# Optimization experiments

Measured on AMD Instinct MI355X. Metric: run time of the kernel, lower is better.

Reference implementation:

```python
import jax, jax.numpy as jnp
import numpy as np
import math

B, T, D = 2, 1024, 4096
H, KVH = 32, 8
HD = D // H            # 128
GROUP = H // KVH       # 4
MAX_SEQ = 4096
ROPE_BASE = 10000.0


def rotate_every_two(x):
    # (x0,x1,x2,x3,...) -> (-x1,x0,-x3,x2,...)
    x1 = x[..., ::2]
    x2 = x[..., 1::2]
    return jnp.stack((-x2, x1), axis=-1).reshape(x.shape)


def build_rope_cache():
    inv_freq = 1.0 / (ROPE_BASE ** (jnp.arange(0, HD, 2, dtype=jnp.float32) / HD))
    t = jnp.arange(MAX_SEQ, dtype=jnp.float32)
    freqs = jnp.einsum('i,j->ij', t, inv_freq)        # (MAX_SEQ, HD/2)
    emb = jnp.concatenate([freqs, freqs], axis=-1)    # (MAX_SEQ, HD) -- matches torch cat([freqs,freqs])
    return jnp.cos(emb), jnp.sin(emb)


def setup_inputs() -> dict:
    key = jax.random.key(0)
    kx, kq, kk, kv, ko = jax.random.split(key, 5)
    x = jax.random.normal(kx, (B, T, D), dtype=jnp.float32)
    # weights stored (in_features, out_features)
    wq = jax.random.normal(kq, (D, H * HD), dtype=jnp.float32) * 0.02
    wk = jax.random.normal(kk, (D, KVH * HD), dtype=jnp.float32) * 0.02
    wv = jax.random.normal(kv, (D, KVH * HD), dtype=jnp.float32) * 0.02
    wo = jax.random.normal(ko, (H * HD, D), dtype=jnp.float32) * 0.02
    return {"x": x, "wq": wq, "wk": wk, "wv": wv, "wo": wo, "start_pos": 0}


def reference(x, wq, wk, wv, wo, start_pos):
    cos_cache, sin_cache = build_rope_cache()
    pos = start_pos + jnp.arange(T)
    cos_t = cos_cache[pos][None, None]   # (1,1,T,HD)
    sin_t = sin_cache[pos][None, None]

    q = (x @ wq).reshape(B, T, H, HD).transpose(0, 2, 1, 3)     # (B,H,T,HD)
    k = (x @ wk).reshape(B, T, KVH, HD).transpose(0, 2, 1, 3)   # (B,KVH,T,HD)
    v = (x @ wv).reshape(B, T, KVH, HD).transpose(0, 2, 1, 3)

    q = q * cos_t + rotate_every_two(q) * sin_t
    k = k * cos_t + rotate_every_two(k) * sin_t

    # GQA: repeat-interleave KV heads to match query heads
    k_exp = jnp.repeat(k, GROUP, axis=1)  # (B,H,T,HD)
    v_exp = jnp.repeat(v, GROUP, axis=1)

    scores = jnp.einsum('bhqd,bhkd->bhqk', q, k_exp) / math.sqrt(HD)
    # causal mask (T_q == T_k here): forbid k > q
    mask = jnp.arange(T)[None, :] > jnp.arange(T)[:, None]
    scores = jnp.where(mask[None, None], -jnp.inf, scores)
    attn = jax.nn.softmax(scores, axis=-1)

    out = jnp.einsum('bhqk,bhkd->bhqd', attn, v_exp)
    out = out.transpose(0, 2, 1, 3).reshape(B, T, H * HD)
    return out @ wo
```

## Files before the change

kernel.cpp:

```cpp
#include <hip/hip_runtime.h>
#include <hip/hip_bf16.h>
#include <math.h>

#define B_    2
#define T_    1024
#define D_    4096
#define H_    32
#define KVH_  8
#define HD_   128
#define GROUP_ 4

static constexpr float SCORE_SCALE = 0.08838834764831845f;

typedef __bf16 bf16x8 __attribute__((ext_vector_type(8)));
typedef float  f32x4  __attribute__((ext_vector_type(4)));
typedef unsigned short u16;

__device__ inline float toF(const __hip_bfloat16 v) { return __bfloat162float(v); }
__device__ inline float toF(const float v)          { return v; }

__device__ inline void storeC(float* p, float v)          { *p = v; }
__device__ inline void storeC(__hip_bfloat16* p, float v) { *p = __float2bfloat16(v); }

__device__ inline unsigned short f2bf(float f) {
    union { float f; unsigned u; } v; v.f = f;
    unsigned r = v.u + 0x7FFFu + ((v.u >> 16) & 1u);
    return (unsigned short)(r >> 16);
}

__device__ inline float bf2f(u16 u) {
    union { float f; unsigned u; } v; v.u = (unsigned)u << 16; return v.f;
}

__device__ inline void gload_lds16(const u16* g, u16* l) {
    __builtin_amdgcn_global_load_lds(
        (const __attribute__((address_space(1))) void*)g,
        (__attribute__((address_space(3))) void*)l, 16, 0, 0);
}


__global__ __launch_bounds__(256) void lconv(const float* __restrict__ S,
                                             u16* __restrict__ D, int n8) {
    int i = blockIdx.x * 256 + threadIdx.x;
    if (i >= n8) return;
    const float4 a = *(const float4*)(S + (size_t)i * 8);
    const float4 b = *(const float4*)(S + (size_t)i * 8 + 4);
    union { int4 v; u16 u[8]; } t;
    t.u[0] = f2bf(a.x); t.u[1] = f2bf(a.y); t.u[2] = f2bf(a.z); t.u[3] = f2bf(a.w);
    t.u[4] = f2bf(b.x); t.u[5] = f2bf(b.y); t.u[6] = f2bf(b.z); t.u[7] = f2bf(b.w);
    *(int4*)(D + (size_t)i * 8) = t.v;
}

template <bool DUAL>
__global__ __launch_bounds__(256) void tconv(const float* __restrict__ S0,
                                             u16* __restrict__ D0,
                                             const float* __restrict__ S1,
                                             u16* __restrict__ D1,
                                             int R, int Cc) {
    const float* __restrict__ S = (DUAL && blockIdx.z) ? S1 : S0;
    u16* __restrict__ D         = (DUAL && blockIdx.z) ? D1 : D0;
    __shared__ u16 Tt[64][72];
    const int tid = threadIdx.x;
    const int r0 = blockIdx.y * 64, c0 = blockIdx.x * 64;
    {
        const int rr = tid >> 4, cc4 = (tid & 15) * 4;
#pragma unroll
        for (int e = 0; e < 4; ++e) {
            const int row = rr + e * 16;
            float4 v = *(const float4*)(S + (size_t)(r0 + row) * Cc + c0 + cc4);
            union { int2 w; u16 u[4]; } t;
            t.u[0] = f2bf(v.x); t.u[1] = f2bf(v.y); t.u[2] = f2bf(v.z); t.u[3] = f2bf(v.w);
            *(int2*)&Tt[row][cc4] = t.w;
        }
    }
    __syncthreads();
    {
        const int cc = tid >> 2, r8 = (tid & 3) * 8;
#pragma unroll
        for (int e = 0; e < 2; ++e) {
            const int rb = r8 + e * 32;
            union { int4 v; u16 u[8]; } t;
#pragma unroll
            for (int j = 0; j < 8; ++j) t.u[j] = Tt[rb + j][cc];
            *(int4*)(D + (size_t)(c0 + cc) * R + r0 + rb) = t.v;
        }
    }
}

template <typename TC, bool DUAL, bool TRC1>
__global__ __launch_bounds__(256, 2) void gemm_bf16(const u16* __restrict__ A,
                                                    const u16* __restrict__ Bt0,
                                                    TC* __restrict__ C0,
                                                    const u16* __restrict__ Bt1,
                                                    TC* __restrict__ C1,
                                                    int M, int N, int K) {
    const u16* __restrict__ Bt = (DUAL && blockIdx.z) ? Bt1 : Bt0;
    TC* __restrict__ C         = (DUAL && blockIdx.z) ? C1 : C0;

    __shared__ u16 As[128 * 32];
    __shared__ u16 Bs[128 * 32];

    const int tid   = threadIdx.x;
    const int lane  = tid & 63;
    const int w     = tid >> 6;
    const int waveM = w >> 1;
    const int waveN = w & 1;
    const int lm    = lane & 15;
    const int quad  = lane >> 4;
    const int bm    = blockIdx.y * 128;
    const int bn    = blockIdx.x * 128;

    const int srow = w * 16 + (lane >> 2);
    const int scol = (lane & 3) * 8;

    const u16* agp0 = A  + (size_t)(bm + srow)      * K + scol;
    const u16* agp1 = A  + (size_t)(bm + srow + 64) * K + scol;
    const u16* bgp0 = Bt + (size_t)(bn + srow)      * K + scol;
    const u16* bgp1 = Bt + (size_t)(bn + srow + 64) * K + scol;

    u16* al0 = &As[(w * 16)      * 32];
    u16* al1 = &As[(w * 16 + 64) * 32];
    u16* bl0 = &Bs[(w * 16)      * 32];
    u16* bl1 = &Bs[(w * 16 + 64) * 32];

    f32x4 acc[4][4];
#pragma unroll
    for (int i = 0; i < 4; ++i)
#pragma unroll
        for (int j = 0; j < 4; ++j) acc[i][j] = (f32x4){0.f, 0.f, 0.f, 0.f};

    for (int k0 = 0; k0 < K; k0 += 32) {
        gload_lds16(agp0 + k0, al0);
        gload_lds16(agp1 + k0, al1);
        gload_lds16(bgp0 + k0, bl0);
        gload_lds16(bgp1 + k0, bl1);
        __syncthreads();

        bf16x8 af[4], bfv[4];
#pragma unroll
        for (int i = 0; i < 4; ++i)
            af[i] = *(const bf16x8*)&As[(waveM * 64 + i * 16 + lm) * 32 + quad * 8];
#pragma unroll
        for (int j = 0; j < 4; ++j)
            bfv[j] = *(const bf16x8*)&Bs[(waveN * 64 + j * 16 + lm) * 32 + quad * 8];
#pragma unroll
        for (int i = 0; i < 4; ++i)
#pragma unroll
            for (int j = 0; j < 4; ++j)
                acc[i][j] = __builtin_amdgcn_mfma_f32_16x16x32_bf16(af[i], bfv[j], acc[i][j], 0, 0, 0);
        __syncthreads();
    }

    if (TRC1 && DUAL && blockIdx.z) {
#pragma unroll
        for (int i = 0; i < 4; ++i) {
            int row0 = bm + waveM * 64 + i * 16 + quad * 4;
#pragma unroll
            for (int j = 0; j < 4; ++j) {
                int col = bn + waveN * 64 + j * 16 + lm;
#pragma unroll
                for (int rr = 0; rr < 4; ++rr)
                    storeC(&C[(size_t)col * M + row0 + rr], acc[i][j][rr]);
            }
        }
    } else {
#pragma unroll
        for (int i = 0; i < 4; ++i) {
            int row0 = bm + waveM * 64 + i * 16 + quad * 4;
#pragma unroll
            for (int j = 0; j < 4; ++j) {
                int col = bn + waveN * 64 + j * 16 + lm;
#pragma unroll
                for (int rr = 0; rr < 4; ++rr)
                    storeC(&C[(size_t)(row0 + rr) * N + col], acc[i][j][rr]);
            }
        }
    }
}

#define LSTR 40

template <typename TA, typename TB, typename TC, bool DUAL, bool TRC1>
__global__ __launch_bounds__(256) void gemm_mfma(const TA* __restrict__ A,
                                                 const TB* __restrict__ B0,
                                                 TC* __restrict__ C0,
                                                 const TB* __restrict__ B1,
                                                 TC* __restrict__ C1,
                                                 int M, int N, int K) {
    const TB* __restrict__ B = (DUAL && blockIdx.z) ? B1 : B0;
    TC* __restrict__ C       = (DUAL && blockIdx.z) ? C1 : C0;

    __shared__ unsigned short As[128 * LSTR];
    __shared__ unsigned short Bs[128 * LSTR];

    const int tid   = threadIdx.x;
    const int lane  = tid & 63;
    const int wv    = tid >> 6;
    const int waveM = wv >> 1;
    const int waveN = wv & 1;
    const int lm    = lane & 15;
    const int quad  = lane >> 4;
    const int bm    = blockIdx.y * 128;
    const int bn    = blockIdx.x * 128;

    f32x4 acc[4][4];
#pragma unroll
    for (int i = 0; i < 4; ++i)
#pragma unroll
        for (int j = 0; j < 4; ++j) acc[i][j] = (f32x4){0.f, 0.f, 0.f, 0.f};

    for (int k0 = 0; k0 < K; k0 += 32) {
#pragma unroll
        for (int e = 0; e < 8; ++e) {
            int p  = tid + e * 256;
            int r  = p >> 4, c2 = (p & 15) * 2;
            const TA* ap = A + (size_t)(bm + r) * K + k0 + c2;
            ushort2 t;
            t.x = f2bf(toF(ap[0]));
            t.y = f2bf(toF(ap[1]));
            *(ushort2*)&As[r * LSTR + c2] = t;
        }
#pragma unroll
        for (int e = 0; e < 8; ++e) {
            int p  = tid + e * 256;
            int n  = p & 127, k2 = (p >> 7) * 2;
            const TB* bp = B + (size_t)(k0 + k2) * N + bn + n;
            ushort2 t;
            t.x = f2bf(toF(bp[0]));
            t.y = f2bf(toF(bp[N]));
            *(ushort2*)&Bs[n * LSTR + k2] = t;
        }
        __syncthreads();

        bf16x8 af[4], bfr[4];
#pragma unroll
        for (int i = 0; i < 4; ++i)
            af[i] = *(const bf16x8*)&As[(waveM * 64 + i * 16 + lm) * LSTR + quad * 8];
#pragma unroll
        for (int j = 0; j < 4; ++j)
            bfr[j] = *(const bf16x8*)&Bs[(waveN * 64 + j * 16 + lm) * LSTR + quad * 8];
#pragma unroll
        for (int i = 0; i < 4; ++i)
#pragma unroll
            for (int j = 0; j < 4; ++j)
                acc[i][j] = __builtin_amdgcn_mfma_f32_16x16x32_bf16(af[i], bfr[j], acc[i][j], 0, 0, 0);
        __syncthreads();
    }

    if (TRC1 && DUAL && blockIdx.z) {
#pragma unroll
        for (int i = 0; i < 4; ++i) {
            int row0 = bm + waveM * 64 + i * 16 + quad * 4;
#pragma unroll
            for (int j = 0; j < 4; ++j) {
                int col = bn + waveN * 64 + j * 16 + lm;
#pragma unroll
                for (int rr = 0; rr < 4; ++rr)
                    storeC(&C[(size_t)col * M + row0 + rr], acc[i][j][rr]);
            }
        }
    } else {
#pragma unroll
        for (int i = 0; i < 4; ++i) {
            int row0 = bm + waveM * 64 + i * 16 + quad * 4;
#pragma unroll
            for (int j = 0; j < 4; ++j) {
                int col = bn + waveN * 64 + j * 16 + lm;
#pragma unroll
                for (int rr = 0; rr < 4; ++rr)
                    storeC(&C[(size_t)(row0 + rr) * N + col], acc[i][j][rr]);
            }
        }
    }
}

__device__ inline void rope_apply8(__hip_bfloat16* p, const float* cs,
                                   const float* sn, int t0) {
    union { int4 v; u16 u[8]; } in, outv;
    in.v = *(const int4*)p;
    float x[8];
#pragma unroll
    for (int i = 0; i < 8; ++i) x[i] = bf2f(in.u[i]);
#pragma unroll
    for (int pr = 0; pr < 4; ++pr) {
        float c0 = cs[t0 + 2 * pr],     s0 = sn[t0 + 2 * pr];
        float c1 = cs[t0 + 2 * pr + 1], s1 = sn[t0 + 2 * pr + 1];
        float e = x[2 * pr], o = x[2 * pr + 1];
        outv.u[2 * pr]     = f2bf(e * c0 - o * s0);
        outv.u[2 * pr + 1] = f2bf(o * c1 + e * s1);
    }
    *(int4*)p = outv.v;
}

__global__ __launch_bounds__(256) void rope_tok(__hip_bfloat16* __restrict__ Q,
                                                __hip_bfloat16* __restrict__ K,
                                                const int* __restrict__ start_pos) {
    __shared__ float cs[64], sn[64];
    const int n   = blockIdx.x;
    const int tid = threadIdx.x;
    const int pos = *start_pos + (n % T_);

    if (tid < 64) {
        float invf = exp2f(-(float)tid * 0.20762050593045232f);
        float ang  = (float)pos * invf;
        float s, c;
        __sincosf(ang, &s, &c);
        s = sinf(ang); c = cosf(ang);
        cs[tid] = c; sn[tid] = s;
    }
    __syncthreads();

    __hip_bfloat16* qrow = Q + (size_t)n * (H_ * HD_);
    __hip_bfloat16* krow = K + (size_t)n * (KVH_ * HD_);
#pragma unroll
    for (int e = 0; e < 2; ++e) {
        int g = tid + e * 256;
        rope_apply8(qrow + g * 8, cs, sn, (g * 8) & 63);
    }
    if (tid < 128)
        rope_apply8(krow + tid * 8, cs, sn, (tid * 8) & 63);
}

template <typename TQ, typename TK>
__global__ __launch_bounds__(256) void rope_kernel(TQ* __restrict__ Q,
                                                   TK* __restrict__ Kt,
                                                   const int* __restrict__ start_pos) {
    int w    = blockIdx.x * 4 + (threadIdx.x >> 6);
    int lane = threadIdx.x & 63;
    int hh = w % (H_ + KVH_);
    int n  = w / (H_ + KVH_);
    int t  = n % T_;
    int pos = *start_pos + t;

    int e0 = 2 * lane, e1 = 2 * lane + 1;
    int j0 = e0 & 63,  j1 = e1 & 63;
    const double LN_BASE = 9.210340371976184;
    double a0 = (double)pos * exp(-((double)(2 * j0) / 128.0) * LN_BASE);
    double a1 = (double)pos * exp(-((double)(2 * j1) / 128.0) * LN_BASE);
    float c0 = (float)cos(a0), s0 = (float)sin(a0);
    float c1 = (float)cos(a1), s1 = (float)sin(a1);

    if (hh < H_) {
        TQ* base = Q + (size_t)n * (H_ * HD_) + hh * HD_;
        float x0 = toF(base[e0]), x1 = toF(base[e1]);
        storeC(&base[e0], x0 * c0 - x1 * s0);
        storeC(&base[e1], x1 * c1 + x0 * s1);
    } else {
        TK* base = Kt + (size_t)n * (KVH_ * HD_) + (hh - H_) * HD_;
        float x0 = toF(base[e0]), x1 = toF(base[e1]);
        storeC(&base[e0], x0 * c0 - x1 * s0);
        storeC(&base[e1], x1 * c1 + x0 * s1);
    }
}

#define KSTR 136
#define VSTR 72
#define PSTR 72

template <typename TQ>
__global__ __launch_bounds__(256, 2) void flash_attn(
        const TQ* __restrict__ Q,
        const __hip_bfloat16* __restrict__ K,
        const __hip_bfloat16* __restrict__ Vt,
        __hip_bfloat16* __restrict__ AO) {
    __shared__ unsigned short Ks[64 * KSTR];
    __shared__ unsigned short Vs[128 * VSTR];
    __shared__ unsigned short Ps[4][16 * PSTR];

    const int tid  = threadIdx.x;
    const int lane = tid & 63;
    const int w    = tid >> 6;
    const int quad = lane >> 4;
    const int lm   = lane & 15;

    const int qt  = (blockIdx.x + blockIdx.y) & 15;
    const int qb  = qt * 64;
    const int h   = blockIdx.y;
    const int b   = blockIdx.z;
    const int kvh = h >> 2;

    const int qw = qb + w * 16;

    bf16x8 qf[4];
    {
        const TQ* qrow = Q + (size_t)(b * T_ + qw + lm) * (H_ * HD_) + h * HD_;
        if constexpr (sizeof(TQ) == 2) {
#pragma unroll
            for (int ks = 0; ks < 4; ++ks)
                qf[ks] = *(const bf16x8*)(qrow + ks * 32 + quad * 8);
        } else {
#pragma unroll
            for (int ks = 0; ks < 4; ++ks) {
                const TQ* p4 = qrow + ks * 32 + quad * 8;
                float4 f0 = *(const float4*)(p4);
                float4 f1 = *(const float4*)(p4 + 4);
                union { bf16x8 v; unsigned short u[8]; } t;
                t.u[0] = f2bf(toF(f0.x)); t.u[1] = f2bf(toF(f0.y));
                t.u[2] = f2bf(toF(f0.z)); t.u[3] = f2bf(toF(f0.w));
                t.u[4] = f2bf(toF(f1.x)); t.u[5] = f2bf(toF(f1.y));
                t.u[6] = f2bf(toF(f1.z)); t.u[7] = f2bf(toF(f1.w));
                qf[ks] = t.v;
            }
        }
    }

    float mI[4], lI[4];
    f32x4 o[8];
#pragma unroll
    for (int rr = 0; rr < 4; ++rr) { mI[rr] = -1e30f; lI[rr] = 0.f; }
#pragma unroll
    for (int dc = 0; dc < 8; ++dc) o[dc] = (f32x4){0.f, 0.f, 0.f, 0.f};

    const int nkt = qt + 1;

    for (int kt = 0; kt < nkt; ++kt) {
        const int t0 = kt * 64;
#pragma unroll
        for (int e = 0; e < 4; ++e) {
            int p = tid + e * 256;
            int tt = p >> 4, d0 = (p & 15) * 8;
            int4 v = *(const int4*)(K + (size_t)(b * T_ + t0 + tt) * (KVH_ * HD_) + kvh * HD_ + d0);
            *(int4*)&Ks[tt * KSTR + d0] = v;
        }
#pragma unroll
        for (int e = 0; e < 4; ++e) {
            int p = tid + e * 256;
            int d = p >> 3, tm = (p & 7) * 8;
            int4 v = *(const int4*)(Vt + (size_t)(kvh * HD_ + d) * (B_ * T_) + b * T_ + t0 + tm);
            *(int4*)&Vs[d * VSTR + tm] = v;
        }
        __syncthreads();

        f32x4 s[4];
#pragma unroll
        for (int tc = 0; tc < 4; ++tc) s[tc] = (f32x4){0.f, 0.f, 0.f, 0.f};
        __builtin_amdgcn_s_setprio(1);
#pragma unroll
        for (int ks = 0; ks < 4; ++ks) {
            bf16x8 kf[4];
#pragma unroll
            for (int tc = 0; tc < 4; ++tc)
                kf[tc] = *(const bf16x8*)&Ks[(tc * 16 + lm) * KSTR + ks * 32 + quad * 8];
#pragma unroll
            for (int tc = 0; tc < 4; ++tc)
                s[tc] = __builtin_amdgcn_mfma_f32_16x16x32_bf16(qf[ks], kf[tc], s[tc], 0, 0, 0);
        }
        __builtin_amdgcn_s_setprio(0);

#pragma unroll
        for (int tc = 0; tc < 4; ++tc)
#pragma unroll
            for (int rr = 0; rr < 4; ++rr) s[tc][rr] *= SCORE_SCALE;

        if (t0 + 63 > qw) {
            int qrow = qw + quad * 4;
#pragma unroll
            for (int tc = 0; tc < 4; ++tc) {
                int tcol = t0 + tc * 16 + lm;
#pragma unroll
                for (int rr = 0; rr < 4; ++rr)
                    if (tcol > qrow + rr) s[tc][rr] = -1e30f;
            }
        }

#pragma unroll
        for (int rr = 0; rr < 4; ++rr) {
            float tmx = fmaxf(fmaxf(s[0][rr], s[1][rr]),
                              fmaxf(s[2][rr], s[3][rr]));
#pragma unroll
            for (int off = 8; off >= 1; off >>= 1)
                tmx = fmaxf(tmx, __shfl_xor(tmx, off, 64));
            float mn    = fmaxf(mI[rr], tmx);
            float alpha = __expf(mI[rr] - mn);
            mI[rr]  = mn;
            float rs = 0.f;
#pragma unroll
            for (int tc = 0; tc < 4; ++tc) {
                float p = __expf(s[tc][rr] - mn);
                s[tc][rr] = p;
                rs += p;
            }
#pragma unroll
            for (int off = 8; off >= 1; off >>= 1)
                rs += __shfl_xor(rs, off, 64);
            lI[rr] = lI[rr] * alpha + rs;
#pragma unroll
            for (int dc = 0; dc < 8; ++dc)
                o[dc][rr] *= alpha;
        }

#pragma unroll
        for (int tc = 0; tc < 4; ++tc)
#pragma unroll
            for (int rr = 0; rr < 4; ++rr)
                Ps[w][(quad * 4 + rr) * PSTR + tc * 16 + lm] = f2bf(s[tc][rr]);

        __builtin_amdgcn_s_setprio(1);
#pragma unroll
        for (int ss = 0; ss < 2; ++ss) {
            bf16x8 pf = *(const bf16x8*)&Ps[w][lm * PSTR + ss * 32 + quad * 8];
#pragma unroll
            for (int dc = 0; dc < 8; ++dc) {
                bf16x8 vf = *(const bf16x8*)&Vs[(dc * 16 + lm) * VSTR + ss * 32 + quad * 8];
                o[dc] = __builtin_amdgcn_mfma_f32_16x16x32_bf16(pf, vf, o[dc], 0, 0, 0);
            }
        }
        __builtin_amdgcn_s_setprio(0);
        __syncthreads();
    }

#pragma unroll
    for (int rr = 0; rr < 4; ++rr) {
        float inv = 1.f / lI[rr];
        size_t row = (size_t)(b * T_ + qw + quad * 4 + rr) * (H_ * HD_) + h * HD_;
#pragma unroll
        for (int dc = 0; dc < 8; ++dc)
            AO[row + dc * 16 + lm] = __float2bfloat16(o[dc][rr] * inv);
    }
}

extern "C" void kernel_launch(void* const* d_in, const int* in_sizes, int n_in,
                              void* d_out, int out_size, void* d_ws, size_t ws_size,
                              hipStream_t stream) {
    const float* x  = (const float*)d_in[0];
    const float* wq = (const float*)d_in[1];
    const float* wk = (const float*)d_in[2];
    const float* wv = (const float*)d_in[3];
    const float* wo = (const float*)d_in[4];
    const int* start_pos = (const int*)d_in[5];
    float* out = (float*)d_out;

    dim3 blk(256);
    const int M   = B_ * T_;
    const int NQ  = H_ * HD_;
    const int NKV = KVH_ * HD_;

    const size_t NEED = 58720256;

    if (ws_size >= NEED) {
        char* w = (char*)d_ws;
        __hip_bfloat16* Kb  = (__hip_bfloat16*)(w);
        __hip_bfloat16* Vtb = (__hip_bfloat16*)(w + (4u  << 20));
        u16*            xb  = (u16*)(w + (8u  << 20));
        __hip_bfloat16* AOb = (__hip_bfloat16*)(w + (8u  << 20));
        u16*            wS  = (u16*)(w + (24u << 20));
        u16* wqb = wS;
        u16* wkb = wS;
        u16* wvb = wS + (size_t)NKV * D_;
        u16* wob = wS;
        __hip_bfloat16* Qb = (__hip_bfloat16*)d_out;

        lconv<<<(M * D_ / 8 + 255) / 256, blk, 0, stream>>>(x, xb, M * D_ / 8);
        tconv<false><<<dim3(NQ / 64, D_ / 64, 1), blk, 0, stream>>>(wq, wqb, nullptr, nullptr, D_, NQ);
        gemm_bf16<__hip_bfloat16, false, false>
            <<<dim3(NQ / 128, M / 128, 1), blk, 0, stream>>>(xb, wqb, Qb, nullptr, nullptr, M, NQ, D_);
        tconv<true><<<dim3(NKV / 64, D_ / 64, 2), blk, 0, stream>>>(wk, wkb, wv, wvb, D_, NKV);
        gemm_bf16<__hip_bfloat16, true, true>
            <<<dim3(NKV / 128, M / 128, 2), blk, 0, stream>>>(xb, wkb, Kb, wvb, Vtb, M, NKV, D_);
        rope_tok<<<M, blk, 0, stream>>>(Qb, Kb, start_pos);
        tconv<false><<<dim3(NQ / 64, NQ / 64, 1), blk, 0, stream>>>(wo, wob, nullptr, nullptr, NQ, D_);
        flash_attn<__hip_bfloat16><<<dim3(T_ / 64, H_, B_), blk, 0, stream>>>(Qb, Kb, Vtb, AOb);
        gemm_bf16<float, false, false>
            <<<dim3(D_ / 128, M / 128, 1), blk, 0, stream>>>((const u16*)AOb, wob, out, nullptr, nullptr, M, D_, NQ);
    } else {
        float* Qf           = out;
        __hip_bfloat16* Kb  = (__hip_bfloat16*)d_ws;
        __hip_bfloat16* Vtb = Kb + (size_t)B_ * T_ * KVH_ * HD_;
        __hip_bfloat16* AOb = Vtb + (size_t)B_ * T_ * KVH_ * HD_;

        gemm_mfma<float, float, float, false, false>
            <<<dim3(NQ / 128, M / 128, 1), blk, 0, stream>>>(x, wq, Qf, nullptr, nullptr, M, NQ, D_);
        gemm_mfma<float, float, __hip_bfloat16, true, true>
            <<<dim3(NKV / 128, M / 128, 2), blk, 0, stream>>>(x, wk, Kb, wv, Vtb, M, NKV, D_);
        rope_kernel<<<(M * (H_ + KVH_)) / 4, blk, 0, stream>>>(Qf, Kb, start_pos);
        flash_attn<float><<<dim3(T_ / 64, H_, B_), blk, 0, stream>>>(Qf, Kb, Vtb, AOb);
        gemm_mfma<__hip_bfloat16, float, float, false, false>
            <<<dim3(D_ / 128, M / 128, 1), blk, 0, stream>>>(AOb, wo, out, nullptr, nullptr, M, D_, NQ);
    }
}
```

Before: 547.5 us.

## Fuse Q/K/V weight conversion and projection GEMMs into single launches

When the workspace is large enough, the three weight transposes/conversions are merged into one tconv3 launch, and the Q, K and V projections run as one 768-block GEMM with a swizzled block-to-tile map. V is written transposed directly in the epilogue. This removes separate launches and tail effects between the Q and KV GEMMs and raises occupancy to 3 blocks per CU. The cost is extra workspace (separate wk/wv buffers) and a fallback path for smaller workspaces. The redundant sincos call in rope is also dropped.

```diff
diff --git a/kernel.cpp b/kernel.cpp
--- a/kernel.cpp
+++ b/kernel.cpp
@@ -87,6 +87,150 @@
     }
 }
 
+__global__ __launch_bounds__(256) void tconv3(const float* __restrict__ wq,
+                                              const float* __restrict__ wk,
+                                              const float* __restrict__ wv,
+                                              u16* __restrict__ dq,
+                                              u16* __restrict__ dk,
+                                              u16* __restrict__ dv) {
+    const int z = blockIdx.z;
+    const float* __restrict__ S;
+    u16* __restrict__ D;
+    int Cc;
+    if (z == 0)      { S = wq; D = dq; Cc = 4096; }
+    else if (z == 1) { S = wk; D = dk; Cc = 1024; }
+    else             { S = wv; D = dv; Cc = 1024; }
+    if (blockIdx.x * 64 >= Cc) return;
+    const int R = 4096;
+
+    __shared__ u16 Tt[64][72];
+    const int tid = threadIdx.x;
+    const int r0 = blockIdx.y * 64, c0 = blockIdx.x * 64;
+    {
+        const int rr = tid >> 4, cc4 = (tid & 15) * 4;
+#pragma unroll
+        for (int e = 0; e < 4; ++e) {
+            const int row = rr + e * 16;
+            float4 v = *(const float4*)(S + (size_t)(r0 + row) * Cc + c0 + cc4);
+            union { int2 w; u16 u[4]; } t;
+            t.u[0] = f2bf(v.x); t.u[1] = f2bf(v.y); t.u[2] = f2bf(v.z); t.u[3] = f2bf(v.w);
+            *(int2*)&Tt[row][cc4] = t.w;
+        }
+    }
+    __syncthreads();
+    {
+        const int cc = tid >> 2, r8 = (tid & 3) * 8;
+#pragma unroll
+        for (int e = 0; e < 2; ++e) {
+            const int rb = r8 + e * 32;
+            union { int4 v; u16 u[8]; } t;
+#pragma unroll
+            for (int j = 0; j < 8; ++j) t.u[j] = Tt[rb + j][cc];
+            *(int4*)(D + (size_t)(c0 + cc) * R + r0 + rb) = t.v;
+        }
+    }
+}
+
+__global__ __launch_bounds__(256, 3) void gemm_qkv(const u16* __restrict__ A,
+                                                   const u16* __restrict__ wqb,
+                                                   const u16* __restrict__ wkb,
+                                                   const u16* __restrict__ wvb,
+                                                   __hip_bfloat16* __restrict__ Qb,
+                                                   __hip_bfloat16* __restrict__ Kb,
+                                                   __hip_bfloat16* __restrict__ Vtb) {
+    const int K = D_;
+    const int M = B_ * T_;
+
+    const int bid = blockIdx.x;
+    const int swz = (bid & 7) * 96 + (bid >> 3);
+
+    const u16* __restrict__ Bt;
+    __hip_bfloat16* __restrict__ C;
+    int bm, bn, N;
+    bool tr;
+    if (swz < 512)      { Bt = wqb; C = Qb;  N = 4096; bm = (swz >> 5) * 128; bn = (swz & 31) * 128; tr = false; }
+    else if (swz < 640) { int i = swz - 512; Bt = wkb; C = Kb;  N = 1024; bm = (i >> 3) * 128; bn = (i & 7) * 128; tr = false; }
+    else                { int i = swz - 640; Bt = wvb; C = Vtb; N = 1024; bm = (i >> 3) * 128; bn = (i & 7) * 128; tr = true; }
+
+    __shared__ u16 As[128 * 32];
+    __shared__ u16 Bs[128 * 32];
+
+    const int tid   = threadIdx.x;
+    const int lane  = tid & 63;
+    const int w     = tid >> 6;
+    const int waveM = w >> 1;
+    const int waveN = w & 1;
+    const int lm    = lane & 15;
+    const int quad  = lane >> 4;
+
+    const int srow = w * 16 + (lane >> 2);
+    const int scol = (lane & 3) * 8;
+
+    const u16* agp0 = A  + (size_t)(bm + srow)      * K + scol;
+    const u16* agp1 = A  + (size_t)(bm + srow + 64) * K + scol;
+    const u16* bgp0 = Bt + (size_t)(bn + srow)      * K + scol;
+    const u16* bgp1 = Bt + (size_t)(bn + srow + 64) * K + scol;
+
+    u16* al0 = &As[(w * 16)      * 32];
+    u16* al1 = &As[(w * 16 + 64) * 32];
+    u16* bl0 = &Bs[(w * 16)      * 32];
+    u16* bl1 = &Bs[(w * 16 + 64) * 32];
+
+    f32x4 acc[4][4];
+#pragma unroll
+    for (int i = 0; i < 4; ++i)
+#pragma unroll
+        for (int j = 0; j < 4; ++j) acc[i][j] = (f32x4){0.f, 0.f, 0.f, 0.f};
+
+    for (int k0 = 0; k0 < K; k0 += 32) {
+        gload_lds16(agp0 + k0, al0);
+        gload_lds16(agp1 + k0, al1);
+        gload_lds16(bgp0 + k0, bl0);
+        gload_lds16(bgp1 + k0, bl1);
+        __syncthreads();
+
+        bf16x8 af[4], bfv[4];
+#pragma unroll
+        for (int i = 0; i < 4; ++i)
+            af[i] = *(const bf16x8*)&As[(waveM * 64 + i * 16 + lm) * 32 + quad * 8];
+#pragma unroll
+        for (int j = 0; j < 4; ++j)
+            bfv[j] = *(const bf16x8*)&Bs[(waveN * 64 + j * 16 + lm) * 32 + quad * 8];
+#pragma unroll
+        for (int i = 0; i < 4; ++i)
+#pragma unroll
+            for (int j = 0; j < 4; ++j)
+                acc[i][j] = __builtin_amdgcn_mfma_f32_16x16x32_bf16(af[i], bfv[j], acc[i][j], 0, 0, 0);
+        __syncthreads();
+    }
+
+    if (tr) {
+#pragma unroll
+        for (int i = 0; i < 4; ++i) {
+            int row0 = bm + waveM * 64 + i * 16 + quad * 4;
+#pragma unroll
+            for (int j = 0; j < 4; ++j) {
+                int col = bn + waveN * 64 + j * 16 + lm;
+#pragma unroll
+                for (int rr = 0; rr < 4; ++rr)
+                    C[(size_t)col * M + row0 + rr] = __float2bfloat16(acc[i][j][rr]);
+            }
+        }
+    } else {
+#pragma unroll
+        for (int i = 0; i < 4; ++i) {
+            int row0 = bm + waveM * 64 + i * 16 + quad * 4;
+#pragma unroll
+            for (int j = 0; j < 4; ++j) {
+                int col = bn + waveN * 64 + j * 16 + lm;
+#pragma unroll
+                for (int rr = 0; rr < 4; ++rr)
+                    C[(size_t)(row0 + rr) * N + col] = __float2bfloat16(acc[i][j][rr]);
+            }
+        }
+    }
+}
+
 template <typename TC, bool DUAL, bool TRC1>
 __global__ __launch_bounds__(256, 2) void gemm_bf16(const u16* __restrict__ A,
                                                     const u16* __restrict__ Bt0,
@@ -303,10 +447,7 @@
     if (tid < 64) {
         float invf = exp2f(-(float)tid * 0.20762050593045232f);
         float ang  = (float)pos * invf;
-        float s, c;
-        __sincosf(ang, &s, &c);
-        s = sinf(ang); c = cosf(ang);
-        cs[tid] = c; sn[tid] = s;
+        cs[tid] = cosf(ang); sn[tid] = sinf(ang);
     }
     __syncthreads();
 
@@ -535,9 +676,30 @@
     const int NQ  = H_ * HD_;
     const int NKV = KVH_ * HD_;
 
-    const size_t NEED = 58720256;
-
-    if (ws_size >= NEED) {
+    const size_t NEED_A = 75497472;
+    const size_t NEED_B = 58720256;
+
+    if (ws_size >= NEED_A) {
+        char* w = (char*)d_ws;
+        __hip_bfloat16* Kb  = (__hip_bfloat16*)(w);
+        __hip_bfloat16* Vtb = (__hip_bfloat16*)(w + (4u  << 20));
+        u16*            xb  = (u16*)(w + (8u  << 20));
+        __hip_bfloat16* AOb = (__hip_bfloat16*)(w + (8u  << 20));
+        u16*            wqb = (u16*)(w + (24u << 20));
+        u16*            wob = (u16*)(w + (24u << 20));
+        u16*            wkb = (u16*)(w + (56u << 20));
+        u16*            wvb = (u16*)(w + (64u << 20));
+        __hip_bfloat16* Qb  = (__hip_bfloat16*)d_out;
+
+        lconv<<<(M * D_ / 8 + 255) / 256, blk, 0, stream>>>(x, xb, M * D_ / 8);
+        tconv3<<<dim3(NQ / 64, D_ / 64, 3), blk, 0, stream>>>(wq, wk, wv, wqb, wkb, wvb);
+        gemm_qkv<<<768, blk, 0, stream>>>(xb, wqb, wkb, wvb, Qb, Kb, Vtb);
+        rope_tok<<<M, blk, 0, stream>>>(Qb, Kb, start_pos);
+        tconv<false><<<dim3(NQ / 64, NQ / 64, 1), blk, 0, stream>>>(wo, wob, nullptr, nullptr, NQ, D_);
+        flash_attn<__hip_bfloat16><<<dim3(T_ / 64, H_, B_), blk, 0, stream>>>(Qb, Kb, Vtb, AOb);
+        gemm_bf16<float, false, false>
+            <<<dim3(D_ / 128, M / 128, 1), blk, 0, stream>>>((const u16*)AOb, wob, out, nullptr, nullptr, M, D_, NQ);
+    } else if (ws_size >= NEED_B) {
         char* w = (char*)d_ws;
         __hip_bfloat16* Kb  = (__hip_bfloat16*)(w);
         __hip_bfloat16* Vtb = (__hip_bfloat16*)(w + (4u  << 20));
```

Result: faster. 495.1 us (-9.6%).
